# Optimization experiments

Measured on AMD Instinct MI355X. Metric: run time of the kernel, lower is better.

## Reference

```python
import jax, jax.numpy as jnp
import numpy as np
from jax.ops import segment_sum, segment_max

N = 100000   # nodes
E = 1600000  # edges
B = 256      # graphs
H = 128      # hidden_channels
F_IN = 4     # input_size
EPS = 1e-5


def _graph_norm(x, w, b, ms, batch):
    # PyG GraphNorm: out = w * (x - ms*mean_g) / sqrt(var_g + eps) + b
    cnt = jnp.maximum(segment_sum(jnp.ones((x.shape[0],), x.dtype), batch, num_segments=B), 1.0)
    mean = segment_sum(x, batch, num_segments=B) / cnt[:, None]
    out = x - mean[batch] * ms
    var = segment_sum(out * out, batch, num_segments=B) / cnt[:, None]
    return w * out / jnp.sqrt(var + EPS)[batch] + b


def _gcn(x, W, b, src, dst):
    # GCNConv with self-loops and symmetric normalization (src/dst already include self-loops)
    h = x @ W                                              # [N, H]
    deg = segment_sum(jnp.ones_like(src, dtype=h.dtype), dst, num_segments=N)
    dinv = jax.lax.rsqrt(jnp.maximum(deg, 1.0))
    norm = dinv[src] * dinv[dst]                           # [E+N]
    return segment_sum(norm[:, None] * h[src], dst, num_segments=N) + b


def _seg_softmax(gate, batch):
    gmax = segment_max(gate, batch, num_segments=B)
    e = jnp.exp(gate - gmax[batch])
    den = segment_sum(e, batch, num_segments=B)
    return e / den[batch]


def setup_inputs() -> dict:
    key = jax.random.key(0)
    ks = jax.random.split(key, 16)
    x = jax.random.normal(ks[0], (N, F_IN), jnp.float32)
    edge_index = jax.random.randint(ks[1], (2, E), 0, N, dtype=jnp.int64)
    batch = jnp.sort(jax.random.randint(ks[2], (N,), 0, B, dtype=jnp.int64))
    r = lambda k, shp, fan: jax.random.normal(k, shp, jnp.float32) / np.sqrt(fan)
    inp = {
        "x": x, "edge_index": edge_index, "batch": batch,
        "W1": r(ks[3], (F_IN, H), F_IN), "b1": jnp.zeros((H,), jnp.float32),
        "W2": r(ks[4], (H, H), H), "b2": jnp.zeros((H,), jnp.float32),
        "W3": r(ks[5], (H, H), H), "b3": jnp.zeros((H,), jnp.float32),
        "gn0_w": jnp.ones((F_IN,), jnp.float32), "gn0_b": jnp.zeros((F_IN,), jnp.float32), "gn0_ms": jnp.ones((F_IN,), jnp.float32),
        "gn1_w": jnp.ones((H,), jnp.float32), "gn1_b": jnp.zeros((H,), jnp.float32), "gn1_ms": jnp.ones((H,), jnp.float32),
        "gn2_w": jnp.ones((H,), jnp.float32), "gn2_b": jnp.zeros((H,), jnp.float32), "gn2_ms": jnp.ones((H,), jnp.float32),
        "gn3_w": jnp.ones((H,), jnp.float32), "gn3_b": jnp.zeros((H,), jnp.float32), "gn3_ms": jnp.ones((H,), jnp.float32),
        "g1": r(ks[6], (H, H), H), "gb1": jnp.zeros((H,), jnp.float32),
        "g2": r(ks[7], (H, H), H), "gb2": jnp.zeros((H,), jnp.float32),
        "g3": r(ks[8], (H, 1), H), "gb3": jnp.zeros((1,), jnp.float32),
        "l1": r(ks[9], (H, H), H), "lb1": jnp.zeros((H,), jnp.float32),
        "l2": r(ks[10], (H, H), H), "lb2": jnp.zeros((H,), jnp.float32),
        "l3": r(ks[11], (H, 1), H), "lb3": jnp.zeros((1,), jnp.float32),
    }
    return inp


def reference(x, edge_index, batch, W1, b1, W2, b2, W3, b3,
              gn0_w, gn0_b, gn0_ms, gn1_w, gn1_b, gn1_ms,
              gn2_w, gn2_b, gn2_ms, gn3_w, gn3_b, gn3_ms,
              g1, gb1, g2, gb2, g3, gb3,
              l1, lb1, l2, lb2, l3, lb3):
    loop = jnp.arange(N, dtype=edge_index.dtype)
    src = jnp.concatenate([edge_index[0], loop])
    dst = jnp.concatenate([edge_index[1], loop])

    h = _graph_norm(x, gn0_w, gn0_b, gn0_ms, batch)
    h = _gcn(h, W1, b1, src, dst)
    h = jax.nn.relu(_graph_norm(h, gn1_w, gn1_b, gn1_ms, batch))
    h = _gcn(h, W2, b2, src, dst)
    h = jax.nn.relu(_graph_norm(h, gn2_w, gn2_b, gn2_ms, batch))
    h = _gcn(h, W3, b3, src, dst)
    h = _graph_norm(h, gn3_w, gn3_b, gn3_ms, batch)

    # GlobalAttention: gate_nn -> scalar gate per node, segment softmax, weighted sum
    g = jax.nn.relu(h @ g1 + gb1)
    g = jax.nn.relu(g @ g2 + gb2)
    gate = g @ g3 + gb3                                   # [N, 1]
    attn = _seg_softmax(gate, batch)                      # [N, 1]
    pooled = segment_sum(attn * h, batch, num_segments=B) # [B, H]

    o = jax.nn.relu(pooled @ l1 + lb1)
    o = jax.nn.relu(o @ l2 + lb2)
    return o @ l3 + lb3                                   # [B, 1]
```

## Files before the change

### kernel.cpp

```cpp
#include <hip/hip_runtime.h>
#include <hip/hip_bf16.h>

#define NN 100000
#define NE 1600000
#define NB 256
#define HD 128
#define EPS 1e-5f
#define NBUK 1563
#define SLOTB 1536
#define EPB 8192
#define MAXG 768

typedef __attribute__((ext_vector_type(8))) short bf16x8v;
typedef __attribute__((ext_vector_type(4))) float f32x4v;

__device__ __forceinline__ float rd_dyn(const void* p, int i, int fflag) {
    if (fflag) {
        unsigned short u = ((const unsigned short*)p)[i];
        return __uint_as_float(((unsigned)u) << 16);
    }
    return ((const float*)p)[i];
}

__device__ __forceinline__ int rd_idx(const int* p, int k, int iflag) {
    return iflag ? p[k] : p[2 * k];
}

__device__ __forceinline__ unsigned short f2bf(float v) {
    __hip_bfloat16 b = __float2bfloat16(v);
    return *(unsigned short*)&b;
}

__device__ __forceinline__ float bflo(unsigned u) { return __uint_as_float(u << 16); }
__device__ __forceinline__ float bfhi(unsigned u) { return __uint_as_float(u & 0xFFFF0000u); }
__device__ __forceinline__ unsigned packbf(float a, float b) {
    return (unsigned)f2bf(a) | ((unsigned)f2bf(b) << 16);
}

__global__ void k_mark7(unsigned short* __restrict__ out, int n) {
    int i = blockIdx.x * blockDim.x + threadIdx.x;
    if (i < n) out[i] = 0x40E0;
}

__global__ void k_detect(const int* __restrict__ batch, const unsigned* __restrict__ w,
                         int* __restrict__ flags, int n) {
    int i = blockIdx.x * blockDim.x + threadIdx.x;
    if (i == 0 && w[0] == 0x3F803F80u) atomicOr(&flags[1], 1);
    if (i < n && (i & 1) && batch[i] != 0) atomicOr(&flags[0], 1);
}

struct CvtArgs {
    const void* p[30];
    int n[30];
    int off[30];
    const void* wp[4];
};
__global__ void k_prep(CvtArgs a, float* __restrict__ out,
                       unsigned short* __restrict__ WT,
                       const int* __restrict__ flagsp,
                       const int* __restrict__ batch,
                       int* __restrict__ start, int* __restrict__ batch32,
                       int* __restrict__ bcur) {
    int j = blockIdx.y;
    int i = blockIdx.x * blockDim.x + threadIdx.x;
    if (j < 30) {
        if (i >= a.n[j]) return;
        out[a.off[j] + i] = rd_dyn(a.p[j], i, flagsp[1]);
    } else if (j < 34) {
        int mat = j - 30;
        if (i >= 16384) return;
        int nidx = i >> 7, k = i & 127;
        WT[mat * 16384 + nidx * 128 + k] = f2bf(rd_dyn(a.wp[mat], k * 128 + nidx, flagsp[1]));
    } else {
        if (i >= NN) return;
        if (i < NBUK) bcur[i] = i * SLOTB;
        int ifl = flagsp[0];
        int b = rd_idx(batch, i, ifl); b = b < 0 ? 0 : (b > NB - 1 ? NB - 1 : b);
        batch32[i] = b;
        int bp;
        if (i == 0) bp = -1;
        else { bp = rd_idx(batch, i - 1, ifl); bp = bp < 0 ? 0 : (bp > NB - 1 ? NB - 1 : bp); }
        for (int g = bp + 1; g <= b; ++g) start[g] = i;
        if (i == NN - 1) { for (int g = b + 1; g <= NB; ++g) start[g] = NN; }
    }
}

__global__ __launch_bounds__(256) void k_bfill(const int* __restrict__ ei,
                                               const int* __restrict__ iflagp,
                                               int* __restrict__ bcur,
                                               unsigned* __restrict__ bkte, int e) {
    __shared__ int lh[NBUK];
    __shared__ int lbase[NBUK];
    int ifl = *iflagp;
    for (int b = threadIdx.x; b < NBUK; b += 256) lh[b] = 0;
    __syncthreads();
    int s0 = blockIdx.x * EPB;
    int s1 = s0 + EPB; if (s1 > e) s1 = e;
    for (int i = s0 + threadIdx.x; i < s1; i += 256) {
        int d = rd_idx(ei, NE + i, ifl);
        int s = rd_idx(ei, i, ifl);
        if ((unsigned)d < (unsigned)NN && (unsigned)s < (unsigned)NN)
            atomicAdd(&lh[d >> 6], 1);
    }
    __syncthreads();
    for (int b = threadIdx.x; b < NBUK; b += 256) {
        int c = lh[b];
        if (c) { lbase[b] = atomicAdd(&bcur[b], c); lh[b] = 0; }
    }
    __syncthreads();
    for (int i = s0 + threadIdx.x; i < s1; i += 256) {
        int d = rd_idx(ei, NE + i, ifl);
        int s = rd_idx(ei, i, ifl);
        if ((unsigned)d < (unsigned)NN && (unsigned)s < (unsigned)NN) {
            int b = d >> 6;
            int li = atomicAdd(&lh[b], 1);
            bkte[lbase[b] + li] = ((unsigned)s << 6) | (unsigned)(d & 63);
        }
    }
}

__global__ __launch_bounds__(256) void k_csrfin_gn4(const unsigned* __restrict__ bkte,
                                                    const int* __restrict__ bcur,
                                                    int* __restrict__ rowptr,
                                                    int* __restrict__ cnt,
                                                    float* __restrict__ dinv,
                                                    int* __restrict__ esrc,
                                                    const void* __restrict__ x,
                                                    const float* __restrict__ w,
                                                    const float* __restrict__ bb,
                                                    const float* __restrict__ ms,
                                                    const int* __restrict__ start,
                                                    const int* __restrict__ fflagp,
                                                    float* __restrict__ out) {
    int t = threadIdx.x;
    if (blockIdx.x < NBUK) {
        __shared__ int lc[64];
        __shared__ int lcur[64];
        int b = blockIdx.x;
        int base = b * 64;
        if (t < 64) lc[t] = 0;
        __syncthreads();
        int r0 = b * SLOTB, r1 = bcur[b];
        for (int j = r0 + t; j < r1; j += 256)
            atomicAdd(&lc[(int)(bkte[j] & 63u)], 1);
        __syncthreads();
        if (t < 64) {
            int v = lc[t];
            int inc = v;
#pragma unroll
            for (int off = 1; off < 64; off <<= 1) {
                int nv = __shfl_up(inc, off, 64);
                if (t >= off) inc += nv;
            }
            int ex = r0 + inc - v;
            lcur[t] = ex;
            int node = base + t;
            if (node < NN) {
                rowptr[node] = ex;
                cnt[node] = v;
                dinv[node] = rsqrtf((float)(v + 1));
            }
        }
        __syncthreads();
        for (int j = r0 + t; j < r1; j += 256) {
            unsigned p = bkte[j];
            int slot = atomicAdd(&lcur[p & 63u], 1);
            esrc[slot] = (int)(p >> 6);
        }
        return;
    }
    __shared__ float4 rs[256], rq[256];
    int g = blockIdx.x - NBUK;
    int s0 = start[g], s1 = start[g + 1];
    if (s1 <= s0) return;
    int ff = *fflagp;
    float cntf = (float)(s1 - s0);
    float sx = 0.f, sy = 0.f, sz = 0.f, sw = 0.f;
    float qx = 0.f, qy = 0.f, qz = 0.f, qw = 0.f;
    for (int n = s0 + t; n < s1; n += 256) {
        float4 v;
        if (ff) {
            uint2 u = ((const uint2*)x)[n];
            v.x = bflo(u.x); v.y = bfhi(u.x); v.z = bflo(u.y); v.w = bfhi(u.y);
        } else {
            v = ((const float4*)x)[n];
        }
        sx += v.x; sy += v.y; sz += v.z; sw += v.w;
        qx = fmaf(v.x, v.x, qx); qy = fmaf(v.y, v.y, qy);
        qz = fmaf(v.z, v.z, qz); qw = fmaf(v.w, v.w, qw);
    }
    rs[t] = make_float4(sx, sy, sz, sw);
    rq[t] = make_float4(qx, qy, qz, qw);
    __syncthreads();
    for (int off = 128; off; off >>= 1) {
        if (t < off) {
            rs[t].x += rs[t + off].x; rs[t].y += rs[t + off].y;
            rs[t].z += rs[t + off].z; rs[t].w += rs[t + off].w;
            rq[t].x += rq[t + off].x; rq[t].y += rq[t + off].y;
            rq[t].z += rq[t + off].z; rq[t].w += rq[t + off].w;
        }
        __syncthreads();
    }
    float4 S = rs[0], Q = rq[0];
    float4 wv = ((const float4*)w)[0];
    float4 bv = ((const float4*)bb)[0];
    float4 mv = ((const float4*)ms)[0];
    float4 mean = make_float4(S.x / cntf, S.y / cntf, S.z / cntf, S.w / cntf);
    float4 sub = make_float4(mean.x * mv.x, mean.y * mv.y, mean.z * mv.z, mean.w * mv.w);
    float4 scale;
    scale.x = wv.x * rsqrtf(Q.x / cntf - 2.f * sub.x * mean.x + sub.x * sub.x + EPS);
    scale.y = wv.y * rsqrtf(Q.y / cntf - 2.f * sub.y * mean.y + sub.y * sub.y + EPS);
    scale.z = wv.z * rsqrtf(Q.z / cntf - 2.f * sub.z * mean.z + sub.z * sub.z + EPS);
    scale.w = wv.w * rsqrtf(Q.w / cntf - 2.f * sub.w * mean.w + sub.w * sub.w + EPS);
    float4* op = (float4*)out;
    for (int n = s0 + t; n < s1; n += 256) {
        float4 v;
        if (ff) {
            uint2 u = ((const uint2*)x)[n];
            v.x = bflo(u.x); v.y = bfhi(u.x); v.z = bflo(u.y); v.w = bfhi(u.y);
        } else {
            v = ((const float4*)x)[n];
        }
        float4 o;
        o.x = scale.x * (v.x - sub.x) + bv.x;
        o.y = scale.y * (v.y - sub.y) + bv.y;
        o.z = scale.z * (v.z - sub.z) + bv.z;
        o.w = scale.w * (v.w - sub.w) + bv.w;
        op[n] = o;
    }
}

__global__ __launch_bounds__(256) void k_gnstats1(const unsigned* __restrict__ Xu,
                                                  const float* __restrict__ w,
                                                  const float* __restrict__ ms,
                                                  const int* __restrict__ start,
                                                  float* __restrict__ SUB,
                                                  float* __restrict__ SCALE) {
    int g = blockIdx.x, seg = blockIdx.y;
    int s0 = start[g], s1 = start[g + 1];
    if (s1 <= s0) return;
    int t = threadIdx.x;
    int wrd = t & 15;
    int p = t >> 4;
    int wbase = seg * 16 + wrd;
    __shared__ float rs0[256], rs1[256], rq0[256], rq1[256];
    float sa = 0.f, sb = 0.f, qa = 0.f, qb = 0.f;
    for (int n = s0 + p; n < s1; n += 16) {
        unsigned u = Xu[(size_t)n * 64 + wbase];
        float lo = bflo(u), hi = bfhi(u);
        sa += lo; qa = fmaf(lo, lo, qa);
        sb += hi; qb = fmaf(hi, hi, qb);
    }
    rs0[t] = sa; rs1[t] = sb; rq0[t] = qa; rq1[t] = qb;
    __syncthreads();
    for (int off = 128; off >= 16; off >>= 1) {
        if (t < off) {
            rs0[t] += rs0[t + off]; rs1[t] += rs1[t + off];
            rq0[t] += rq0[t + off]; rq1[t] += rq1[t + off];
        }
        __syncthreads();
    }
    if (t < 16) {
        float cnt = (float)(s1 - s0);
        int c0 = 2 * (seg * 16 + t), c1 = c0 + 1;
        float mean0 = rs0[t] / cnt, mean1 = rs1[t] / cnt;
        float sub0 = mean0 * ms[c0], sub1 = mean1 * ms[c1];
        float var0 = rq0[t] / cnt - 2.f * sub0 * mean0 + sub0 * sub0;
        float var1 = rq1[t] / cnt - 2.f * sub1 * mean1 + sub1 * sub1;
        SUB[g * 128 + c0] = sub0; SUB[g * 128 + c1] = sub1;
        SCALE[g * 128 + c0] = w[c0] * rsqrtf(var0 + EPS);
        SCALE[g * 128 + c1] = w[c1] * rsqrtf(var1 + EPS);
    }
}

__global__ __launch_bounds__(256) void k_gather4gemm(const int* __restrict__ rowptr,
                                                     const int* __restrict__ cnt,
                                                     const int* __restrict__ esrc,
                                                     const float* __restrict__ dinv,
                                                     const float* __restrict__ h0,
                                                     const float* __restrict__ W1,
                                                     const float* __restrict__ b1,
                                                     unsigned* __restrict__ Xu) {
    __shared__ float w1s[512];
    __shared__ float b1s[128];
    int tid = threadIdx.x;
    w1s[tid] = W1[tid];
    w1s[256 + tid] = W1[256 + tid];
    if (tid < 128) b1s[tid] = b1[tid];
    __syncthreads();
    int node = blockIdx.x * 4 + (tid >> 6);
    int lane = tid & 63;
    if (node >= NN) return;
    int ch = lane & 3;
    int r0 = rowptr[node], r1 = r0 + cnt[node];
    float acc = 0.f;
    for (int j = r0 + (lane >> 2); j < r1; j += 16) {
        int s = esrc[j];
        acc = fmaf(dinv[s], h0[s * 4 + ch], acc);
    }
#pragma unroll
    for (int mask = 4; mask <= 32; mask <<= 1)
        acc += __shfl_xor(acc, mask, 64);
    float dd = dinv[node];
    float z = dd * acc + dd * dd * h0[node * 4 + ch];
    float za = __shfl(z, 0, 64), zb = __shfl(z, 1, 64);
    float zc = __shfl(z, 2, 64), zd = __shfl(z, 3, 64);
    int c0 = 2 * lane, c1 = 2 * lane + 1;
    float v0 = za * w1s[c0] + zb * w1s[128 + c0] + zc * w1s[256 + c0] + zd * w1s[384 + c0] + b1s[c0];
    float v1 = za * w1s[c1] + zb * w1s[128 + c1] + zc * w1s[256 + c1] + zd * w1s[384 + c1] + b1s[c1];
    Xu[node * 64 + lane] = packbf(v0, v1);
}

__global__ __launch_bounds__(256) void k_gemm_mfma_bf(const unsigned* __restrict__ Xu,
                                                      const int* __restrict__ batch32,
                                                      const float* __restrict__ SUB,
                                                      const float* __restrict__ SCALE,
                                                      const float* __restrict__ gnb,
                                                      int relu,
                                                      const unsigned short* __restrict__ WT,
                                                      const float* __restrict__ dinv,
                                                      unsigned short* __restrict__ out) {
    __shared__ unsigned short xs[16][136];
    int base = blockIdx.x * 16;
    int tid = threadIdx.x;
    for (int idx = tid; idx < 1024; idx += 256) {
        int r = idx >> 6, cp = idx & 63;
        int g = batch32[base + r];
        unsigned u = Xu[(base + r) * 64 + cp];
        float2 sub = ((const float2*)(SUB + g * 128))[cp];
        float2 sc  = ((const float2*)(SCALE + g * 128))[cp];
        float2 gb  = ((const float2*)gnb)[cp];
        float va = (bflo(u) - sub.x) * sc.x + gb.x;
        float vb = (bfhi(u) - sub.y) * sc.y + gb.y;
        if (relu) { va = fmaxf(va, 0.f); vb = fmaxf(vb, 0.f); }
        xs[r][2 * cp] = f2bf(va);
        xs[r][2 * cp + 1] = f2bf(vb);
    }
    __syncthreads();
    int wave = tid >> 6, lane = tid & 63;
    int m = lane & 15, quad = lane >> 4;
    f32x4v acc0 = {0.f, 0.f, 0.f, 0.f}, acc1 = {0.f, 0.f, 0.f, 0.f};
    int c0 = wave * 32 + m, c1 = c0 + 16;
#pragma unroll
    for (int kk = 0; kk < 4; ++kk) {
        int ko = kk * 32 + quad * 8;
        bf16x8v a  = *(const bf16x8v*)&xs[m][ko];
        bf16x8v b0 = *(const bf16x8v*)&WT[c0 * 128 + ko];
        bf16x8v b1 = *(const bf16x8v*)&WT[c1 * 128 + ko];
        acc0 = __builtin_amdgcn_mfma_f32_16x16x32_bf16(a, b0, acc0, 0, 0, 0);
        acc1 = __builtin_amdgcn_mfma_f32_16x16x32_bf16(a, b1, acc1, 0, 0, 0);
    }
#pragma unroll
    for (int reg = 0; reg < 4; ++reg) {
        int row = base + quad * 4 + reg;
        float dv = dinv[row];
        out[row * 128 + c0] = f2bf(dv * acc0[reg]);
        out[row * 128 + c1] = f2bf(dv * acc1[reg]);
    }
}

#define ACC4(u) do { \
    a0 += bflo((u).x); a1 += bfhi((u).x); \
    a2 += bflo((u).y); a3 += bfhi((u).y); \
    a4 += bflo((u).z); a5 += bfhi((u).z); \
    a6 += bflo((u).w); a7 += bfhi((u).w); } while (0)

__global__ __launch_bounds__(256) void k_gather_bf(const int* __restrict__ rowptr,
                                                   const int* __restrict__ cnt,
                                                   const int* __restrict__ esrc,
                                                   const float* __restrict__ dinv,
                                                   const unsigned* __restrict__ h,
                                                   const float* __restrict__ bias,
                                                   unsigned* __restrict__ Xu) {
    int node = blockIdx.x * 4 + (threadIdx.x >> 6);
    int lane = threadIdx.x & 63;
    if (node >= NN) return;
    int q = lane >> 4, s = lane & 15;
    int r0 = rowptr[node], r1 = r0 + cnt[node];
    const uint4* hp = (const uint4*)h;
    float a0 = 0.f, a1 = 0.f, a2 = 0.f, a3 = 0.f;
    float a4 = 0.f, a5 = 0.f, a6 = 0.f, a7 = 0.f;
    int j = r0 + q;
    for (; j + 12 < r1; j += 16) {
        int e0 = esrc[j], e1 = esrc[j + 4], e2 = esrc[j + 8], e3 = esrc[j + 12];
        uint4 u0 = hp[e0 * 16 + s];
        uint4 u1 = hp[e1 * 16 + s];
        uint4 u2 = hp[e2 * 16 + s];
        uint4 u3 = hp[e3 * 16 + s];
        ACC4(u0); ACC4(u1); ACC4(u2); ACC4(u3);
    }
    for (; j + 4 < r1; j += 8) {
        int e0 = esrc[j], e1 = esrc[j + 4];
        uint4 u0 = hp[e0 * 16 + s];
        uint4 u1 = hp[e1 * 16 + s];
        ACC4(u0); ACC4(u1);
    }
    for (; j < r1; j += 4) {
        int e0 = esrc[j];
        uint4 u0 = hp[e0 * 16 + s];
        ACC4(u0);
    }
    a0 += __shfl_xor(a0, 16, 64); a0 += __shfl_xor(a0, 32, 64);
    a1 += __shfl_xor(a1, 16, 64); a1 += __shfl_xor(a1, 32, 64);
    a2 += __shfl_xor(a2, 16, 64); a2 += __shfl_xor(a2, 32, 64);
    a3 += __shfl_xor(a3, 16, 64); a3 += __shfl_xor(a3, 32, 64);
    a4 += __shfl_xor(a4, 16, 64); a4 += __shfl_xor(a4, 32, 64);
    a5 += __shfl_xor(a5, 16, 64); a5 += __shfl_xor(a5, 32, 64);
    a6 += __shfl_xor(a6, 16, 64); a6 += __shfl_xor(a6, 32, 64);
    a7 += __shfl_xor(a7, 16, 64); a7 += __shfl_xor(a7, 32, 64);
    int cp = 4 * s + q;
    float ax = q == 0 ? a0 : q == 1 ? a2 : q == 2 ? a4 : a6;
    float ay = q == 0 ? a1 : q == 1 ? a3 : q == 2 ? a5 : a7;
    float dd = dinv[node];
    unsigned us = h[node * 64 + cp];
    float2 bb = ((const float2*)bias)[cp];
    float ox = dd * (ax + bflo(us)) + bb.x;
    float oy = dd * (ay + bfhi(us)) + bb.y;
    Xu[node * 64 + cp] = packbf(ox, oy);
}

__global__ __launch_bounds__(256) void k_gate_fused(const unsigned* __restrict__ Xu,
                                                    const int* __restrict__ batch32,
                                                    const float* __restrict__ SUB,
                                                    const float* __restrict__ SCALE,
                                                    const float* __restrict__ gnb,
                                                    const unsigned short* __restrict__ GT1,
                                                    const float* __restrict__ gb1,
                                                    const unsigned short* __restrict__ GT2,
                                                    const float* __restrict__ gb2,
                                                    const float* __restrict__ g3,
                                                    const float* __restrict__ gb3,
                                                    float* __restrict__ gate) {
    __shared__ unsigned short xs[16][136];
    __shared__ unsigned short t1[16][136];
    __shared__ float redw[64];
    int base = blockIdx.x * 16;
    int tid = threadIdx.x;
    for (int idx = tid; idx < 1024; idx += 256) {
        int r = idx >> 6, cp = idx & 63;
        int g = batch32[base + r];
        unsigned u = Xu[(base + r) * 64 + cp];
        float2 sub = ((const float2*)(SUB + g * 128))[cp];
        float2 sc  = ((const float2*)(SCALE + g * 128))[cp];
        float2 gb  = ((const float2*)gnb)[cp];
        xs[r][2 * cp] = f2bf((bflo(u) - sub.x) * sc.x + gb.x);
        xs[r][2 * cp + 1] = f2bf((bfhi(u) - sub.y) * sc.y + gb.y);
    }
    __syncthreads();
    int wave = tid >> 6, lane = tid & 63;
    int m = lane & 15, quad = lane >> 4;
    int c0 = wave * 32 + m, c1 = c0 + 16;
    f32x4v acc0 = {0.f, 0.f, 0.f, 0.f}, acc1 = {0.f, 0.f, 0.f, 0.f};
#pragma unroll
    for (int kk = 0; kk < 4; ++kk) {
        int ko = kk * 32 + quad * 8;
        bf16x8v a  = *(const bf16x8v*)&xs[m][ko];
        bf16x8v b0 = *(const bf16x8v*)&GT1[c0 * 128 + ko];
        bf16x8v b1 = *(const bf16x8v*)&GT1[c1 * 128 + ko];
        acc0 = __builtin_amdgcn_mfma_f32_16x16x32_bf16(a, b0, acc0, 0, 0, 0);
        acc1 = __builtin_amdgcn_mfma_f32_16x16x32_bf16(a, b1, acc1, 0, 0, 0);
    }
    float bj0 = gb1[c0], bj1 = gb1[c1];
#pragma unroll
    for (int reg = 0; reg < 4; ++reg) {
        int row = quad * 4 + reg;
        t1[row][c0] = f2bf(fmaxf(acc0[reg] + bj0, 0.f));
        t1[row][c1] = f2bf(fmaxf(acc1[reg] + bj1, 0.f));
    }
    __syncthreads();
    f32x4v d0 = {0.f, 0.f, 0.f, 0.f}, d1 = {0.f, 0.f, 0.f, 0.f};
#pragma unroll
    for (int kk = 0; kk < 4; ++kk) {
        int ko = kk * 32 + quad * 8;
        bf16x8v a  = *(const bf16x8v*)&t1[m][ko];
        bf16x8v b0 = *(const bf16x8v*)&GT2[c0 * 128 + ko];
        bf16x8v b1 = *(const bf16x8v*)&GT2[c1 * 128 + ko];
        d0 = __builtin_amdgcn_mfma_f32_16x16x32_bf16(a, b0, d0, 0, 0, 0);
        d1 = __builtin_amdgcn_mfma_f32_16x16x32_bf16(a, b1, d1, 0, 0, 0);
    }
    float g30 = g3[c0], g31 = g3[c1];
    float bk0 = gb2[c0], bk1 = gb2[c1];
    float contrib[4];
#pragma unroll
    for (int reg = 0; reg < 4; ++reg) {
        float v0 = fmaxf(d0[reg] + bk0, 0.f);
        float v1 = fmaxf(d1[reg] + bk1, 0.f);
        contrib[reg] = v0 * g30 + v1 * g31;
    }
#pragma unroll
    for (int mask = 1; mask <= 8; mask <<= 1) {
#pragma unroll
        for (int reg = 0; reg < 4; ++reg)
            contrib[reg] += __shfl_xor(contrib[reg], mask, 64);
    }
    if (m == 0) {
#pragma unroll
        for (int reg = 0; reg < 4; ++reg)
            redw[wave * 16 + quad * 4 + reg] = contrib[reg];
    }
    __syncthreads();
    if (tid < 16) {
        float s = redw[tid] + redw[16 + tid] + redw[32 + tid] + redw[48 + tid];
        gate[base + tid] = s + gb3[0];
    }
}

__global__ __launch_bounds__(256) void k_smpool_head(const unsigned* __restrict__ Xu,
                                                     const float* __restrict__ SUB,
                                                     const float* __restrict__ SCALE,
                                                     const float* __restrict__ gnb,
                                                     const float* __restrict__ gate,
                                                     const int* __restrict__ start,
                                                     const float* __restrict__ l1, const float* __restrict__ lb1,
                                                     const float* __restrict__ l2, const float* __restrict__ lb2,
                                                     const float* __restrict__ l3, const float* __restrict__ lb3,
                                                     const int* __restrict__ fflagp,
                                                     void* __restrict__ out) {
    int g = blockIdx.x, t = threadIdx.x;
    __shared__ float red[256];
    __shared__ float att[MAXG];
    __shared__ float4 rs4[256];
    __shared__ float pool[128];
    __shared__ float o[128];
    int s0 = start[g], s1 = start[g + 1];
    int len = s1 - s0;
    bool fits = len <= MAXG;
    float m = -1e30f;
    for (int i = s0 + t; i < s1; i += 256) m = fmaxf(m, gate[i]);
    red[t] = m; __syncthreads();
    for (int off = 128; off; off >>= 1) { if (t < off) red[t] = fmaxf(red[t], red[t + off]); __syncthreads(); }
    m = red[0]; __syncthreads();
    float sden = 0.f;
    for (int i = s0 + t; i < s1; i += 256) {
        float e = expf(gate[i] - m);
        if (fits) att[i - s0] = e;
        sden += e;
    }
    red[t] = sden; __syncthreads();
    for (int off = 128; off; off >>= 1) { if (t < off) red[t] += red[t + off]; __syncthreads(); }
    float invden = len > 0 ? 1.f / red[0] : 0.f;
    __syncthreads();
    int cp2 = t & 31, p = t >> 5;
    float4 sb4 = {0.f, 0.f, 0.f, 0.f}, sc4 = {0.f, 0.f, 0.f, 0.f}, gb4 = {0.f, 0.f, 0.f, 0.f};
    if (len > 0) {
        sb4 = ((const float4*)(SUB + g * 128))[cp2];
        sc4 = ((const float4*)(SCALE + g * 128))[cp2];
        gb4 = ((const float4*)gnb)[cp2];
    }
    float a0 = 0.f, a1 = 0.f, a2 = 0.f, a3 = 0.f;
    for (int n = s0 + p; n < s1; n += 8) {
        float a = (fits ? att[n - s0] : expf(gate[n] - m)) * invden;
        uint2 u = ((const uint2*)(Xu + (size_t)n * 64))[cp2];
        a0 += a * ((bflo(u.x) - sb4.x) * sc4.x + gb4.x);
        a1 += a * ((bfhi(u.x) - sb4.y) * sc4.y + gb4.y);
        a2 += a * ((bflo(u.y) - sb4.z) * sc4.z + gb4.z);
        a3 += a * ((bfhi(u.y) - sb4.w) * sc4.w + gb4.w);
    }
    rs4[t] = make_float4(a0, a1, a2, a3);
    __syncthreads();
    for (int off = 128; off >= 32; off >>= 1) {
        if (t < off) {
            rs4[t].x += rs4[t + off].x; rs4[t].y += rs4[t + off].y;
            rs4[t].z += rs4[t + off].z; rs4[t].w += rs4[t + off].w;
        }
        __syncthreads();
    }
    if (t < 32) {
        pool[4 * t]     = rs4[t].x;
        pool[4 * t + 1] = rs4[t].y;
        pool[4 * t + 2] = rs4[t].z;
        pool[4 * t + 3] = rs4[t].w;
    }
    __syncthreads();
    if (t < 128) {
        float a = 0.f;
        for (int k = 0; k < 128; ++k) a += pool[k] * l1[k * 128 + t];
        o[t] = fmaxf(a + lb1[t], 0.f);
    }
    __syncthreads();
    if (t < 128) {
        float b = 0.f;
        for (int k = 0; k < 128; ++k) b += o[k] * l2[k * 128 + t];
        b = fmaxf(b + lb2[t], 0.f);
        red[t] = b * l3[t];
    }
    __syncthreads();
    for (int off = 64; off; off >>= 1) { if (t < off) red[t] += red[t + off]; __syncthreads(); }
    if (t == 0) {
        float r = red[0] + lb3[0];
        if (*fflagp) ((__hip_bfloat16*)out)[g] = __float2bfloat16(r);
        else ((float*)out)[g] = r;
    }
}

extern "C" void kernel_launch(void* const* d_in, const int* in_sizes, int n_in,
                              void* d_out, int out_size, void* d_ws, size_t ws_size,
                              hipStream_t stream) {
    const void* x = d_in[0];
    const int* ei_raw = (const int*)d_in[1];
    const int* batch_raw = (const int*)d_in[2];
    (void)n_in; (void)out_size;

    char* ws = (char*)d_ws;
    size_t off = 0;
    auto alloc = [&](size_t bytes) -> void* {
        void* p = ws + off;
        off += (bytes + 255) & ~(size_t)255;
        return p;
    };
    unsigned* Xu  = (unsigned*)alloc((size_t)NN * HD * 2);
    float* Y      = (float*)alloc((size_t)NN * HD * 4);
    float* h0     = (float*)alloc((size_t)NN * 4 * 4);
    float* dinv   = (float*)alloc((size_t)NN * 4);
    float* gate   = (float*)alloc((size_t)NN * 4);
    int*   start  = (int*)alloc((size_t)(NB + 1) * 4);
    int*   batch32= (int*)alloc((size_t)NN * 4);
    float* P      = (float*)alloc((size_t)131072 * 4);
    unsigned short* WT = (unsigned short*)alloc((size_t)4 * 16384 * 2);
    float* SUB    = (float*)alloc((size_t)NB * HD * 4);
    float* SCALE  = (float*)alloc((size_t)NB * HD * 4);
    int*   flags  = (int*)alloc(256);
    int*   rowptr = (int*)alloc((size_t)NN * 4);
    int*   cnt    = (int*)alloc((size_t)NN * 4);
    int*   esrc   = (int*)alloc((size_t)NBUK * SLOTB * 4);
    int*   bcur   = (int*)alloc((size_t)NBUK * 4);
    unsigned* bkte = (unsigned*)(Y + (size_t)NN * HD / 2);

    if (ws_size < off) {
        k_mark7<<<1, 256, 0, stream>>>((unsigned short*)d_out, NB);
        return;
    }

    int* iflag = flags;
    int* fflag = flags + 1;
    hipMemsetAsync(flags, 0, 8, stream);
    k_detect<<<(NN + 255) / 256, 256, 0, stream>>>(batch_raw, (const unsigned*)d_in[12], flags, NN);

    CvtArgs ca;
    float* fp[33];
    {
        int poff = 0;
        for (int i = 3; i < 33; ++i) {
            int n = in_sizes[i];
            ca.p[i - 3] = d_in[i];
            ca.n[i - 3] = n;
            ca.off[i - 3] = poff;
            fp[i] = P + poff;
            poff += n;
        }
        ca.wp[0] = d_in[5];
        ca.wp[1] = d_in[7];
        ca.wp[2] = d_in[21];
        ca.wp[3] = d_in[23];
    }
    {
        dim3 grid((NN + 255) / 256, 35);
        k_prep<<<grid, 256, 0, stream>>>(ca, P, WT, flags, batch_raw, start, batch32, bcur);
    }
    const float *W1 = fp[3], *b1 = fp[4], *b2 = fp[6], *b3 = fp[8];
    const float *gn0w = fp[9],  *gn0b = fp[10], *gn0m = fp[11];
    const float *gn1w = fp[12], *gn1m = fp[14], *gn1b = fp[13];
    const float *gn2w = fp[15], *gn2b = fp[16], *gn2m = fp[17];
    const float *gn3w = fp[18], *gn3b = fp[19], *gn3m = fp[20];
    const float *gb1 = fp[22], *gb2 = fp[24], *g3 = fp[25], *gb3 = fp[26];
    const float *l1 = fp[27], *lb1 = fp[28], *l2 = fp[29], *lb2 = fp[30], *l3 = fp[31], *lb3 = fp[32];

    const unsigned short* WT2 = WT;
    const unsigned short* WT3 = WT + 16384;
    const unsigned short* GT1 = WT + 2 * 16384;
    const unsigned short* GT2 = WT + 3 * 16384;

    int ebg = (NE + EPB - 1) / EPB;
    k_bfill<<<ebg, 256, 0, stream>>>(ei_raw, iflag, bcur, bkte, NE);
    k_csrfin_gn4<<<NBUK + NB, 256, 0, stream>>>(bkte, bcur, rowptr, cnt, dinv, esrc,
                                                x, gn0w, gn0b, gn0m, start, fflag, h0);

    k_gather4gemm<<<(NN + 3) / 4, 256, 0, stream>>>(rowptr, cnt, esrc, dinv, h0, W1, b1, Xu);

    unsigned short* Yb = (unsigned short*)Y;
    dim3 sgrid(NB, 4);

    k_gnstats1<<<sgrid, 256, 0, stream>>>(Xu, gn1w, gn1m, start, SUB, SCALE);
    k_gemm_mfma_bf<<<NN / 16, 256, 0, stream>>>(Xu, batch32, SUB, SCALE, gn1b, 1, WT2, dinv, Yb);
    k_gather_bf<<<(NN + 3) / 4, 256, 0, stream>>>(rowptr, cnt, esrc, dinv, (const unsigned*)Yb, b2, Xu);

    k_gnstats1<<<sgrid, 256, 0, stream>>>(Xu, gn2w, gn2m, start, SUB, SCALE);
    k_gemm_mfma_bf<<<NN / 16, 256, 0, stream>>>(Xu, batch32, SUB, SCALE, gn2b, 1, WT3, dinv, Yb);
    k_gather_bf<<<(NN + 3) / 4, 256, 0, stream>>>(rowptr, cnt, esrc, dinv, (const unsigned*)Yb, b3, Xu);

    k_gnstats1<<<sgrid, 256, 0, stream>>>(Xu, gn3w, gn3m, start, SUB, SCALE);
    k_gate_fused<<<NN / 16, 256, 0, stream>>>(Xu, batch32, SUB, SCALE, gn3b,
                                              GT1, gb1, GT2, gb2, g3, gb3, gate);
    k_smpool_head<<<NB, 256, 0, stream>>>(Xu, SUB, SCALE, gn3b, gate, start,
                                          l1, lb1, l2, lb2, l3, lb3, fflag, d_out);
}
```

Baseline: 539.4 us.

## Split attention pooling across chunked blocks and move MLP head to separate kernel

The fused softmax-pool-head kernel, which ran one block per graph, is split into a pooling kernel with eight blocks per graph. Each block recomputes the graph's softmax max and denominator, then pools a chunk of nodes into partial sums. A separate head kernel reduces the partials and runs the MLP. This exposes more parallelism for the 256 graphs at the cost of redundant softmax reductions and an extra launch. The edge-bucket fill block size EPB also drops from 8192 to 2048, giving more blocks in k_bfill.

```diff
diff --git a/kernel.cpp b/kernel.cpp
--- a/kernel.cpp
+++ b/kernel.cpp
@@ -8,8 +8,8 @@
 #define EPS 1e-5f
 #define NBUK 1563
 #define SLOTB 1536
-#define EPB 8192
-#define MAXG 768
+#define EPB 2048
+#define NCHK 8
 
 typedef __attribute__((ext_vector_type(8))) short bf16x8v;
 typedef __attribute__((ext_vector_type(4))) float f32x4v;
@@ -505,86 +505,78 @@
     }
 }
 
-__global__ __launch_bounds__(256) void k_smpool_head(const unsigned* __restrict__ Xu,
-                                                     const float* __restrict__ SUB,
-                                                     const float* __restrict__ SCALE,
-                                                     const float* __restrict__ gnb,
-                                                     const float* __restrict__ gate,
-                                                     const int* __restrict__ start,
-                                                     const float* __restrict__ l1, const float* __restrict__ lb1,
-                                                     const float* __restrict__ l2, const float* __restrict__ lb2,
-                                                     const float* __restrict__ l3, const float* __restrict__ lb3,
-                                                     const int* __restrict__ fflagp,
-                                                     void* __restrict__ out) {
-    int g = blockIdx.x, t = threadIdx.x;
+__global__ __launch_bounds__(256) void k_smpool(const unsigned* __restrict__ Xu,
+                                                const float* __restrict__ SUB,
+                                                const float* __restrict__ SCALE,
+                                                const float* __restrict__ gnb,
+                                                const float* __restrict__ gate,
+                                                const int* __restrict__ start,
+                                                float* __restrict__ PP) {
+    int g = blockIdx.x, kk = blockIdx.y;
+    int s0 = start[g], s1 = start[g + 1];
+    int t = threadIdx.x;
     __shared__ float red[256];
-    __shared__ float att[MAXG];
-    __shared__ float4 rs4[256];
-    __shared__ float pool[128];
-    __shared__ float o[128];
-    int s0 = start[g], s1 = start[g + 1];
-    int len = s1 - s0;
-    bool fits = len <= MAXG;
+    __shared__ float r0s[256], r1s[256];
+    if (s1 <= s0) {
+        if (t < 64) {
+            int bidx = (g * NCHK + kk) * 128;
+            ((float2*)(PP + bidx))[t] = make_float2(0.f, 0.f);
+        }
+        return;
+    }
     float m = -1e30f;
     for (int i = s0 + t; i < s1; i += 256) m = fmaxf(m, gate[i]);
     red[t] = m; __syncthreads();
     for (int off = 128; off; off >>= 1) { if (t < off) red[t] = fmaxf(red[t], red[t + off]); __syncthreads(); }
     m = red[0]; __syncthreads();
     float sden = 0.f;
-    for (int i = s0 + t; i < s1; i += 256) {
-        float e = expf(gate[i] - m);
-        if (fits) att[i - s0] = e;
-        sden += e;
-    }
+    for (int i = s0 + t; i < s1; i += 256) sden += expf(gate[i] - m);
     red[t] = sden; __syncthreads();
     for (int off = 128; off; off >>= 1) { if (t < off) red[t] += red[t + off]; __syncthreads(); }
-    float invden = len > 0 ? 1.f / red[0] : 0.f;
-    __syncthreads();
-    int cp2 = t & 31, p = t >> 5;
-    float4 sb4 = {0.f, 0.f, 0.f, 0.f}, sc4 = {0.f, 0.f, 0.f, 0.f}, gb4 = {0.f, 0.f, 0.f, 0.f};
-    if (len > 0) {
-        sb4 = ((const float4*)(SUB + g * 128))[cp2];
-        sc4 = ((const float4*)(SCALE + g * 128))[cp2];
-        gb4 = ((const float4*)gnb)[cp2];
-    }
-    float a0 = 0.f, a1 = 0.f, a2 = 0.f, a3 = 0.f;
-    for (int n = s0 + p; n < s1; n += 8) {
-        float a = (fits ? att[n - s0] : expf(gate[n] - m)) * invden;
-        uint2 u = ((const uint2*)(Xu + (size_t)n * 64))[cp2];
-        a0 += a * ((bflo(u.x) - sb4.x) * sc4.x + gb4.x);
-        a1 += a * ((bfhi(u.x) - sb4.y) * sc4.y + gb4.y);
-        a2 += a * ((bflo(u.y) - sb4.z) * sc4.z + gb4.z);
-        a3 += a * ((bfhi(u.y) - sb4.w) * sc4.w + gb4.w);
-    }
-    rs4[t] = make_float4(a0, a1, a2, a3);
-    __syncthreads();
-    for (int off = 128; off >= 32; off >>= 1) {
-        if (t < off) {
-            rs4[t].x += rs4[t + off].x; rs4[t].y += rs4[t + off].y;
-            rs4[t].z += rs4[t + off].z; rs4[t].w += rs4[t + off].w;
-        }
-        __syncthreads();
-    }
-    if (t < 32) {
-        pool[4 * t]     = rs4[t].x;
-        pool[4 * t + 1] = rs4[t].y;
-        pool[4 * t + 2] = rs4[t].z;
-        pool[4 * t + 3] = rs4[t].w;
-    }
-    __syncthreads();
-    if (t < 128) {
-        float a = 0.f;
-        for (int k = 0; k < 128; ++k) a += pool[k] * l1[k * 128 + t];
-        o[t] = fmaxf(a + lb1[t], 0.f);
-    }
-    __syncthreads();
-    if (t < 128) {
-        float b = 0.f;
-        for (int k = 0; k < 128; ++k) b += o[k] * l2[k * 128 + t];
-        b = fmaxf(b + lb2[t], 0.f);
-        red[t] = b * l3[t];
-    }
-    __syncthreads();
+    float invden = 1.f / red[0];
+    int len = (s1 - s0 + NCHK - 1) / NCHK;
+    int c0 = s0 + kk * len, c1 = c0 + len; if (c1 > s1) c1 = s1;
+    int cp = t & 63, p = t >> 6;
+    float2 sub = ((const float2*)(SUB + g * 128))[cp];
+    float2 sc  = ((const float2*)(SCALE + g * 128))[cp];
+    float2 gb  = ((const float2*)gnb)[cp];
+    float sa = 0.f, sb = 0.f;
+    for (int n = c0 + p; n < c1; n += 4) {
+        float a = expf(gate[n] - m) * invden;
+        unsigned u = Xu[n * 64 + cp];
+        sa += a * ((bflo(u) - sub.x) * sc.x + gb.x);
+        sb += a * ((bfhi(u) - sub.y) * sc.y + gb.y);
+    }
+    r0s[t] = sa; r1s[t] = sb; __syncthreads();
+    if (p == 0) {
+        int bidx = (g * NCHK + kk) * 128;
+        float2 o;
+        o.x = r0s[cp] + r0s[64 + cp] + r0s[128 + cp] + r0s[192 + cp];
+        o.y = r1s[cp] + r1s[64 + cp] + r1s[128 + cp] + r1s[192 + cp];
+        ((float2*)(PP + bidx))[cp] = o;
+    }
+}
+
+__global__ __launch_bounds__(128) void k_head(const float* __restrict__ PP,
+                                              const float* __restrict__ l1, const float* __restrict__ lb1,
+                                              const float* __restrict__ l2, const float* __restrict__ lb2,
+                                              const float* __restrict__ l3, const float* __restrict__ lb3,
+                                              const int* __restrict__ fflagp,
+                                              void* __restrict__ out) {
+    int g = blockIdx.x, t = threadIdx.x;
+    __shared__ float p[128], o[128], red[128];
+    float s = 0.f;
+#pragma unroll
+    for (int k = 0; k < NCHK; ++k) s += PP[(g * NCHK + k) * 128 + t];
+    p[t] = s; __syncthreads();
+    float a = 0.f;
+    for (int k = 0; k < 128; ++k) a += p[k] * l1[k * 128 + t];
+    a = fmaxf(a + lb1[t], 0.f);
+    o[t] = a; __syncthreads();
+    float b = 0.f;
+    for (int k = 0; k < 128; ++k) b += o[k] * l2[k * 128 + t];
+    b = fmaxf(b + lb2[t], 0.f);
+    red[t] = b * l3[t]; __syncthreads();
     for (int off = 64; off; off >>= 1) { if (t < off) red[t] += red[t + off]; __syncthreads(); }
     if (t == 0) {
         float r = red[0] + lb3[0];
@@ -619,6 +611,7 @@
     unsigned short* WT = (unsigned short*)alloc((size_t)4 * 16384 * 2);
     float* SUB    = (float*)alloc((size_t)NB * HD * 4);
     float* SCALE  = (float*)alloc((size_t)NB * HD * 4);
+    float* PP     = (float*)alloc((size_t)NB * NCHK * 128 * 4);
     int*   flags  = (int*)alloc(256);
     int*   rowptr = (int*)alloc((size_t)NN * 4);
     int*   cnt    = (int*)alloc((size_t)NN * 4);
@@ -679,6 +672,7 @@
 
     unsigned short* Yb = (unsigned short*)Y;
     dim3 sgrid(NB, 4);
+    dim3 pgrid(NB, NCHK);
 
     k_gnstats1<<<sgrid, 256, 0, stream>>>(Xu, gn1w, gn1m, start, SUB, SCALE);
     k_gemm_mfma_bf<<<NN / 16, 256, 0, stream>>>(Xu, batch32, SUB, SCALE, gn1b, 1, WT2, dinv, Yb);
@@ -691,6 +685,6 @@
     k_gnstats1<<<sgrid, 256, 0, stream>>>(Xu, gn3w, gn3m, start, SUB, SCALE);
     k_gate_fused<<<NN / 16, 256, 0, stream>>>(Xu, batch32, SUB, SCALE, gn3b,
                                               GT1, gb1, GT2, gb2, g3, gb3, gate);
-    k_smpool_head<<<NB, 256, 0, stream>>>(Xu, SUB, SCALE, gn3b, gate, start,
-                                          l1, lb1, l2, lb2, l3, lb3, fflag, d_out);
-}
+    k_smpool<<<pgrid, 256, 0, stream>>>(Xu, SUB, SCALE, gn3b, gate, start, PP);
+    k_head<<<NB, 128, 0, stream>>>(PP, l1, lb1, l2, lb2, l3, lb3, fflag, d_out);
+}
```

Measured after the change: 542.8 us. No clear change (+0.6%).
